# Kernel tuning notes

Hardware: AMD Instinct MI355X
Metric: run time of the kernel (lower is better)

Reference implementation:

```python
import jax, jax.numpy as jnp
import numpy as np

IN_DIM = 64
OUT_DIM = 64
NUM_HEADS = 4
NEG_SLOPE = 0.2
GAMMA = 1.0  # constraint_gamma
NUM_VARS = 100000
NUM_CLAUSES = 100000
NUM_CLUSTERS = 2048
VARS_PER = 64
CLAUSES_PER = 64
NUM_EDGES = 400000


def _xavier(k, shape):
    bound = np.sqrt(6.0 / (shape[0] + shape[1])).astype(np.float32)
    return jax.random.uniform(k, shape, jnp.float32, -bound, bound)


def setup_inputs() -> dict:
    key = jax.random.key(0)
    ks = jax.random.split(key, 11)
    return {
        "x_var": jax.random.normal(ks[0], (NUM_VARS, IN_DIM), jnp.float32),
        "x_clause": jax.random.normal(ks[1], (NUM_CLAUSES, IN_DIM), jnp.float32),
        "var_clause_edge_index": jax.random.randint(ks[2], (2, NUM_EDGES), 0, NUM_VARS),
        "edge_polarity": jax.random.normal(ks[3], (NUM_EDGES, 1), jnp.float32),
        "cluster_var_ids": jax.random.randint(ks[4], (NUM_CLUSTERS, VARS_PER), 0, NUM_VARS),
        "cluster_clause_ids": jax.random.randint(ks[5], (NUM_CLUSTERS, CLAUSES_PER), 0, NUM_CLAUSES),
        "satisfaction_scores": jax.random.uniform(ks[6], (NUM_CLAUSES,), jnp.float32),
        "active_heads": 4,
        "W_Q": _xavier(ks[7], (OUT_DIM, IN_DIM)),
        "W_K": _xavier(ks[8], (OUT_DIM, IN_DIM)),
        "W_V": _xavier(ks[9], (OUT_DIM, IN_DIM)),
        "head_weights": jnp.ones((NUM_HEADS,), jnp.float32),
        "out_proj_w": _xavier(ks[10], (OUT_DIM, OUT_DIM)),
        "out_proj_b": jnp.zeros((OUT_DIM,), jnp.float32),
    }


def reference(x_var, x_clause, var_clause_edge_index, edge_polarity,
              cluster_var_ids, cluster_clause_ids, satisfaction_scores,
              active_heads, W_Q, W_K, W_V, head_weights, out_proj_w, out_proj_b):
    # NOTE: var_clause_edge_index / edge_polarity are accepted but unused,
    # matching the original forward body.
    num_vars = x_var.shape[0]
    x_all = jnp.concatenate([x_var, x_clause], axis=0)            # [N, D]
    Q = x_all @ W_Q.T
    K = x_all @ W_K.T
    V = x_all @ W_V.T

    # Block-diagonal cluster layout: [C, S] with S = VARS_PER + CLAUSES_PER
    nodes = jnp.concatenate([cluster_var_ids, cluster_clause_ids + num_vars], axis=1)
    Qc = Q[nodes]                                                 # [C, S, D]
    Kc = K[nodes]
    Vc = V[nodes]

    scale = jnp.asarray(np.sqrt(OUT_DIM), Qc.dtype)
    scores = jnp.einsum('csd,ctd->cst', Qc, Kc) / scale            # [C, S, S]
    # constraint-aware bias on clause columns (added before leaky_relu)
    bias = jnp.concatenate(
        [jnp.zeros(cluster_var_ids.shape, scores.dtype),
         GAMMA * satisfaction_scores[cluster_clause_ids]], axis=1)  # [C, S]
    scores = jax.nn.leaky_relu(scores + bias[:, None, :], NEG_SLOPE)
    attn = jax.nn.softmax(scores, axis=-1)

    head_w = jnp.mean(head_weights[:active_heads])
    h = jnp.einsum('cst,ctd->csd', attn, Vc) * head_w             # [C, S, D]

    flat = nodes.reshape(-1)
    out = jnp.zeros_like(x_all).at[flat].add(h.reshape(-1, OUT_DIM))
    count = jnp.zeros((x_all.shape[0],), x_all.dtype).at[flat].add(1.0)
    out = out / jnp.maximum(count, 1.0)[:, None]
    out = out @ out_proj_w.T + out_proj_b

    return (x_var + out[:num_vars], x_clause + out[num_vars:])
```

## Files before the change

kernel.cpp:

```cpp
#include <hip/hip_runtime.h>


#define NV 100000
#define NN 200000
#define NCLUST 2048
#define XS 72

typedef __attribute__((ext_vector_type(8))) short short8;
typedef __attribute__((ext_vector_type(4))) unsigned uint4v;
typedef __attribute__((ext_vector_type(16))) float floatx16;

__device__ __forceinline__ unsigned short f2bf(float f) {
    union { float f; unsigned u; } v; v.f = f;
    unsigned r = v.u + 0x7fffu + ((v.u >> 16) & 1u);
    return (unsigned short)(r >> 16);
}
__device__ __forceinline__ unsigned pack2bf(float lo, float hi) {
    union { float f; unsigned u; } a, b; a.f = lo; b.f = hi;
    unsigned ra = a.u + 0x7fffu + ((a.u >> 16) & 1u);
    unsigned rb = b.u + 0x7fffu + ((b.u >> 16) & 1u);
    return (ra >> 16) | (rb & 0xffff0000u);
}
__device__ __forceinline__ int crow(int r, int lane) {
    return (r & 3) + 8 * (r >> 2) + 4 * (lane >> 5);
}

__global__ __launch_bounds__(256) void prep_kernel(
    const float* __restrict__ WQ, const float* __restrict__ WK,
    const float* __restrict__ WV, const float* __restrict__ Wout,
    const float* __restrict__ head_weights, const int* __restrict__ active_heads_p,
    unsigned short* __restrict__ Mtr, unsigned short* __restrict__ Pbf)
{
    int o = blockIdx.x * blockDim.x + threadIdx.x;
    int ah = active_heads_p[0];
    float hw = 0.f;
    for (int i = 0; i < ah; ++i) hw += head_weights[i];
    hw /= (float)ah;
    if (o < 4096) {
        int d = o >> 6, a = o & 63;
        float acc = 0.f;
        for (int j = 0; j < 64; ++j) acc += WQ[j*64 + a] * WK[j*64 + d];
        Mtr[o] = f2bf(acc * 0.125f);
    } else if (o < 8192) {
        int o2 = o - 4096;
        int j = o2 >> 6, b = o2 & 63;
        float acc = 0.f;
        for (int d = 0; d < 64; ++d) acc += Wout[j*64 + d] * WV[d*64 + b];
        Pbf[o2] = f2bf(acc * hw);
    }
}

__device__ __forceinline__ void cluster_compute(
    unsigned short* Xc, unsigned short* Eh,
    const int* ids, const float* biascl,
    const unsigned short* __restrict__ Mtr,
    unsigned short* __restrict__ accum_bf,
    int lane, int w, int m, int hk)
{
    {
        floatx16 z0 = {}, z1 = {};
        #pragma unroll
        for (int ks = 0; ks < 4; ++ks) {
            short8 mb0 = *(const short8*)(Mtr + m * 64 + ks * 16 + hk);
            short8 mb1 = *(const short8*)(Mtr + (32 + m) * 64 + ks * 16 + hk);
            short8 a = *(const short8*)&Xc[(w * 32 + m) * XS + ks * 16 + hk];
            z0 = __builtin_amdgcn_mfma_f32_32x32x16_bf16(a, mb0, z0, 0, 0, 0);
            z1 = __builtin_amdgcn_mfma_f32_32x32x16_bf16(a, mb1, z1, 0, 0, 0);
        }
        #pragma unroll
        for (int r = 0; r < 16; ++r) {
            int row = w * 32 + crow(r, lane);
            Eh[row * XS + m]      = f2bf(z0[r]);
            Eh[row * XS + 32 + m] = f2bf(z1[r]);
        }
    }

    floatx16 sc[4] = {{}, {}, {}, {}};
    #pragma unroll
    for (int ks = 0; ks < 4; ++ks) {
        short8 a = *(const short8*)&Eh[(w * 32 + m) * XS + ks * 16 + hk];
        #pragma unroll
        for (int nt = 0; nt < 4; ++nt) {
            short8 b = *(const short8*)&Xc[(nt * 32 + m) * XS + ks * 16 + hk];
            sc[nt] = __builtin_amdgcn_mfma_f32_32x32x16_bf16(a, b, sc[nt], 0, 0, 0);
        }
    }

    const float b2 = biascl[m], b3 = biascl[32 + m];
    #pragma unroll
    for (int r = 0; r < 16; ++r) {
        float a0 = sc[0][r], a1 = sc[1][r], a2 = sc[2][r] + b2, a3 = sc[3][r] + b3;
        a0 = a0 > 0.f ? a0 : 0.2f * a0;
        a1 = a1 > 0.f ? a1 : 0.2f * a1;
        a2 = a2 > 0.f ? a2 : 0.2f * a2;
        a3 = a3 > 0.f ? a3 : 0.2f * a3;
        a0 = __expf(a0); a1 = __expf(a1); a2 = __expf(a2); a3 = __expf(a3);
        float s4 = (a0 + a1) + (a2 + a3);
        #pragma unroll
        for (int off = 1; off < 32; off <<= 1) s4 += __shfl_xor(s4, off, 64);
        float inv = __builtin_amdgcn_rcpf(s4);
        sc[0][r] = a0 * inv; sc[1][r] = a1 * inv;
        sc[2][r] = a2 * inv; sc[3][r] = a3 * inv;
    }

    #pragma unroll
    for (int r = 0; r < 16; ++r) {
        int row = w * 32 + crow(r, lane);
        Eh[row * XS + m]      = f2bf(sc[0][r]);
        Eh[row * XS + 32 + m] = f2bf(sc[1][r]);
    }

    floatx16 g0 = {}, g1 = {};
    #pragma unroll
    for (int ks = 0; ks < 4; ++ks) {
        short8 a = *(const short8*)&Eh[(w * 32 + m) * XS + ks * 16 + hk];
        short8 b0, b1;
        #pragma unroll
        for (int j = 0; j < 8; ++j) {
            int t = ks * 16 + hk + j;
            b0[j] = (short)Xc[t * XS + m];
            b1[j] = (short)Xc[t * XS + 32 + m];
        }
        g0 = __builtin_amdgcn_mfma_f32_32x32x16_bf16(a, b0, g0, 0, 0, 0);
        g1 = __builtin_amdgcn_mfma_f32_32x32x16_bf16(a, b1, g1, 0, 0, 0);
    }

    #pragma unroll
    for (int r = 0; r < 16; ++r) {
        int row = w * 32 + crow(r, lane);
        Eh[row * XS + m]      = f2bf(sc[2][r]);
        Eh[row * XS + 32 + m] = f2bf(sc[3][r]);
    }

    #pragma unroll
    for (int ks = 0; ks < 4; ++ks) {
        short8 a = *(const short8*)&Eh[(w * 32 + m) * XS + ks * 16 + hk];
        short8 b0, b1;
        #pragma unroll
        for (int j = 0; j < 8; ++j) {
            int t = 64 + ks * 16 + hk + j;
            b0[j] = (short)Xc[t * XS + m];
            b1[j] = (short)Xc[t * XS + 32 + m];
        }
        g0 = __builtin_amdgcn_mfma_f32_32x32x16_bf16(a, b0, g0, 0, 0, 0);
        g1 = __builtin_amdgcn_mfma_f32_32x32x16_bf16(a, b1, g1, 0, 0, 0);
    }

    const bool ev = !(lane & 1);
    const int colbase = ev ? m : (31 + m);
    #pragma unroll
    for (int r = 0; r < 16; ++r) {
        int row = w * 32 + crow(r, lane);
        int nid = ids[row];
        float a0 = g0[r], a1 = g1[r];
        float t0 = __shfl_xor(a0, 1, 64);
        float t1 = __shfl_xor(a1, 1, 64);
        float lo = ev ? a0 : t1;
        float hi = ev ? t0 : a1;
        unsigned pk = (unsigned)f2bf(lo) | ((unsigned)f2bf(hi) << 16);
        unsigned long long addr =
            (unsigned long long)(accum_bf + (size_t)nid * 64 + colbase);
        asm volatile("global_atomic_pk_add_bf16 %0, %1, off"
                     :: "v"(addr), "v"(pk) : "memory");
    }
}

__global__ __launch_bounds__(256, 3) void attn_kernel(
    const float* __restrict__ x_var, const float* __restrict__ x_clause,
    const int* __restrict__ cvar, const int* __restrict__ ccl,
    const float* __restrict__ sat, const unsigned short* __restrict__ Mtr,
    unsigned short* __restrict__ accum_bf, float* __restrict__ countv)
{
    __shared__ unsigned short Xc[128 * XS];
    __shared__ unsigned short Eh[128 * XS];
    __shared__ unsigned stage4[16 * 256];
    __shared__ int   ids[128];
    __shared__ float biascl[64];

    const int tid = threadIdx.x, lane = tid & 63, w = tid >> 6;
    const int m = lane & 31, hk = (lane >> 5) * 8;
    const int c0 = blockIdx.x * 2;
    const int r = tid >> 1, half = tid & 1;

    int nid0, nid1;
    const float *src0, *src1;
    float satv0 = 0.f, satv1 = 0.f;
    if (r < 64) {
        nid0 = cvar[c0 * 64 + r];
        nid1 = cvar[c0 * 64 + 64 + r];
        src0 = x_var + (size_t)nid0 * 64;
        src1 = x_var + (size_t)nid1 * 64;
    } else {
        int cid0 = ccl[c0 * 64 + (r - 64)];
        int cid1 = ccl[c0 * 64 + r];
        nid0 = NV + cid0; nid1 = NV + cid1;
        src0 = x_clause + (size_t)cid0 * 64;
        src1 = x_clause + (size_t)cid1 * 64;
        if (half) { satv0 = sat[cid0]; satv1 = sat[cid1]; }
    }

    const float4* s40 = (const float4*)src0 + half * 8;
    const float4* s41 = (const float4*)src1 + half * 8;
    float4 v0[8], v1[8];
    #pragma unroll
    for (int i = 0; i < 8; ++i) v0[i] = s40[i];
    #pragma unroll
    for (int i = 0; i < 8; ++i) v1[i] = s41[i];

    if (!half) atomicAdd(&countv[nid0], 1.0f);

    {
        union { unsigned u[16]; short8 v[4]; } hb;
        #pragma unroll
        for (int i = 0; i < 8; ++i) {
            hb.u[2*i]   = pack2bf(v0[i].x, v0[i].y);
            hb.u[2*i+1] = pack2bf(v0[i].z, v0[i].w);
        }
        const int cb = half * 32;
        #pragma unroll
        for (int i = 0; i < 4; ++i) *(short8*)&Xc[r * XS + cb + i * 8] = hb.v[i];
    }
    #pragma unroll
    for (int i = 0; i < 8; ++i) {
        stage4[(2*i)   * 256 + tid] = pack2bf(v1[i].x, v1[i].y);
        stage4[(2*i+1) * 256 + tid] = pack2bf(v1[i].z, v1[i].w);
    }
    if (!half) ids[r] = nid0;
    if (r >= 64 && half) biascl[r - 64] = satv0;
    __syncthreads();

    cluster_compute(Xc, Eh, ids, biascl, Mtr, accum_bf, lane, w, m, hk);
    __syncthreads();

    {
        const int cb = half * 32;
        #pragma unroll
        for (int j = 0; j < 4; ++j) {
            uint4v t;
            #pragma unroll
            for (int q = 0; q < 4; ++q) t[q] = stage4[(4*j + q) * 256 + tid];
            *(uint4v*)&Xc[r * XS + cb + 8 * j] = t;
        }
    }
    if (!half) { ids[r] = nid1; atomicAdd(&countv[nid1], 1.0f); }
    if (r >= 64 && half) biascl[r - 64] = satv1;
    __syncthreads();

    cluster_compute(Xc, Eh, ids, biascl, Mtr, accum_bf, lane, w, m, hk);
}

__global__ __launch_bounds__(256, 4) void finalize_kernel(
    const float* __restrict__ x_var, const float* __restrict__ x_clause,
    const unsigned short* __restrict__ accum_bf, const float* __restrict__ countv,
    const unsigned short* __restrict__ Pbf, const float* __restrict__ bout,
    float* __restrict__ out)
{
    __shared__ float cnts[128];
    const int tid = threadIdx.x, lane = tid & 63, w = tid >> 6;
    const int base = blockIdx.x * 128;
    if (tid < 128) {
        int n = base + tid;
        cnts[tid] = (n < NN) ? countv[n] : 1.f;
    }
    __syncthreads();

    const int m = lane & 31, hk = (lane >> 5) * 8;
    short8 pb[2][4];
    #pragma unroll
    for (int nt = 0; nt < 2; ++nt)
        #pragma unroll
        for (int ks = 0; ks < 4; ++ks)
            pb[nt][ks] = *(const short8*)(Pbf + (nt * 32 + m) * 64 + ks * 16 + hk);
    const float bias0 = bout[m], bias1 = bout[32 + m];

    const unsigned short* arow = accum_bf + (size_t)(base + w * 32 + m) * 64;
    floatx16 c0 = {}, c1 = {};
    #pragma unroll
    for (int ks = 0; ks < 4; ++ks) {
        short8 a = *(const short8*)(arow + ks * 16 + hk);
        c0 = __builtin_amdgcn_mfma_f32_32x32x16_bf16(a, pb[0][ks], c0, 0, 0, 0);
        c1 = __builtin_amdgcn_mfma_f32_32x32x16_bf16(a, pb[1][ks], c1, 0, 0, 0);
    }
    #pragma unroll
    for (int r = 0; r < 16; ++r) {
        int lrow = w * 32 + crow(r, lane);
        int n = base + lrow;
        if (n < NN) {
            float inv = 1.0f / fmaxf(cnts[lrow], 1.0f);
            const float* xs = (n < NV) ? (x_var + (size_t)n * 64)
                                       : (x_clause + (size_t)(n - NV) * 64);
            out[(size_t)n * 64 + m]      = xs[m]      + c0[r] * inv + bias0;
            out[(size_t)n * 64 + 32 + m] = xs[32 + m] + c1[r] * inv + bias1;
        }
    }
}

extern "C" void kernel_launch(void* const* d_in, const int* in_sizes, int n_in,
                              void* d_out, int out_size, void* d_ws, size_t ws_size,
                              hipStream_t stream)
{
    const float* x_var        = (const float*)d_in[0];
    const float* x_clause     = (const float*)d_in[1];
    const int*   cvar         = (const int*)d_in[4];
    const int*   ccl          = (const int*)d_in[5];
    const float* sat          = (const float*)d_in[6];
    const int*   active_heads = (const int*)d_in[7];
    const float* WQ           = (const float*)d_in[8];
    const float* WK           = (const float*)d_in[9];
    const float* WV           = (const float*)d_in[10];
    const float* head_weights = (const float*)d_in[11];
    const float* Wout         = (const float*)d_in[12];
    const float* bout         = (const float*)d_in[13];

    unsigned short* accum_bf = (unsigned short*)d_ws;
    float* countv = (float*)(accum_bf + (size_t)NN * 64);
    unsigned short* Mtr = (unsigned short*)(countv + NN);
    unsigned short* Pbf = Mtr + 4096;

    hipMemsetAsync(accum_bf, 0, (size_t)NN * 64 * 2 + (size_t)NN * 4, stream);
    prep_kernel<<<32, 256, 0, stream>>>(WQ, WK, WV, Wout, head_weights, active_heads, Mtr, Pbf);
    attn_kernel<<<NCLUST / 2, 256, 0, stream>>>(x_var, x_clause, cvar, ccl, sat, Mtr, accum_bf, countv);
    finalize_kernel<<<(NN + 127) / 128, 256, 0, stream>>>(x_var, x_clause, accum_bf, countv, Pbf, bout, (float*)d_out);
}
```

Baseline: 217.5 us.

## Ping-pong LDS buffers across two clusters, drop staging buffer, double finalize tile

The attention kernel drops the separate stage4 LDS staging area. The second cluster's bf16 features are kept in registers and written into the first cluster's scratch buffer near the end of the first cluster's compute, so the two LDS buffers swap roles. This cuts shared memory per block and lets launch bounds request 4 blocks per CU instead of 3. One full __syncthreads is replaced by a lighter LDS-only barrier. The finalize kernel now handles 256 rows per block with two M-tiles per wave, which halves the grid and reuses the loaded Pbf fragments. The risk is higher register pressure from the carried vectors, which may spill at the tighter occupancy target.

```diff
diff --git a/kernel.cpp b/kernel.cpp
--- a/kernel.cpp
+++ b/kernel.cpp
@@ -7,7 +7,6 @@
 #define XS 72
 
 typedef __attribute__((ext_vector_type(8))) short short8;
-typedef __attribute__((ext_vector_type(4))) unsigned uint4v;
 typedef __attribute__((ext_vector_type(16))) float floatx16;
 
 __device__ __forceinline__ unsigned short f2bf(float f) {
@@ -23,6 +22,12 @@
 }
 __device__ __forceinline__ int crow(int r, int lane) {
     return (r & 3) + 8 * (r >> 2) + 4 * (lane >> 5);
+}
+__device__ __forceinline__ void bar_lds() {
+    __builtin_amdgcn_sched_barrier(0);
+    asm volatile("s_waitcnt lgkmcnt(0)" ::: "memory");
+    __builtin_amdgcn_s_barrier();
+    __builtin_amdgcn_sched_barrier(0);
 }
 
 __global__ __launch_bounds__(256) void prep_kernel(
@@ -50,12 +55,14 @@
     }
 }
 
+template<bool WN>
 __device__ __forceinline__ void cluster_compute(
-    unsigned short* Xc, unsigned short* Eh,
+    unsigned short* X, unsigned short* E,
     const int* ids, const float* biascl,
     const unsigned short* __restrict__ Mtr,
     unsigned short* __restrict__ accum_bf,
-    int lane, int w, int m, int hk)
+    int lane, int w, int m, int hk, int r, int cb,
+    short8 nx0, short8 nx1, short8 nx2, short8 nx3)
 {
     {
         floatx16 z0 = {}, z1 = {};
@@ -63,33 +70,33 @@
         for (int ks = 0; ks < 4; ++ks) {
             short8 mb0 = *(const short8*)(Mtr + m * 64 + ks * 16 + hk);
             short8 mb1 = *(const short8*)(Mtr + (32 + m) * 64 + ks * 16 + hk);
-            short8 a = *(const short8*)&Xc[(w * 32 + m) * XS + ks * 16 + hk];
+            short8 a = *(const short8*)&X[(w * 32 + m) * XS + ks * 16 + hk];
             z0 = __builtin_amdgcn_mfma_f32_32x32x16_bf16(a, mb0, z0, 0, 0, 0);
             z1 = __builtin_amdgcn_mfma_f32_32x32x16_bf16(a, mb1, z1, 0, 0, 0);
         }
         #pragma unroll
-        for (int r = 0; r < 16; ++r) {
-            int row = w * 32 + crow(r, lane);
-            Eh[row * XS + m]      = f2bf(z0[r]);
-            Eh[row * XS + 32 + m] = f2bf(z1[r]);
+        for (int rr = 0; rr < 16; ++rr) {
+            int row = w * 32 + crow(rr, lane);
+            E[row * XS + m]      = f2bf(z0[rr]);
+            E[row * XS + 32 + m] = f2bf(z1[rr]);
         }
     }
 
     floatx16 sc[4] = {{}, {}, {}, {}};
     #pragma unroll
     for (int ks = 0; ks < 4; ++ks) {
-        short8 a = *(const short8*)&Eh[(w * 32 + m) * XS + ks * 16 + hk];
+        short8 a = *(const short8*)&E[(w * 32 + m) * XS + ks * 16 + hk];
         #pragma unroll
         for (int nt = 0; nt < 4; ++nt) {
-            short8 b = *(const short8*)&Xc[(nt * 32 + m) * XS + ks * 16 + hk];
+            short8 b = *(const short8*)&X[(nt * 32 + m) * XS + ks * 16 + hk];
             sc[nt] = __builtin_amdgcn_mfma_f32_32x32x16_bf16(a, b, sc[nt], 0, 0, 0);
         }
     }
 
     const float b2 = biascl[m], b3 = biascl[32 + m];
     #pragma unroll
-    for (int r = 0; r < 16; ++r) {
-        float a0 = sc[0][r], a1 = sc[1][r], a2 = sc[2][r] + b2, a3 = sc[3][r] + b3;
+    for (int rr = 0; rr < 16; ++rr) {
+        float a0 = sc[0][rr], a1 = sc[1][rr], a2 = sc[2][rr] + b2, a3 = sc[3][rr] + b3;
         a0 = a0 > 0.f ? a0 : 0.2f * a0;
         a1 = a1 > 0.f ? a1 : 0.2f * a1;
         a2 = a2 > 0.f ? a2 : 0.2f * a2;
@@ -99,60 +106,67 @@
         #pragma unroll
         for (int off = 1; off < 32; off <<= 1) s4 += __shfl_xor(s4, off, 64);
         float inv = __builtin_amdgcn_rcpf(s4);
-        sc[0][r] = a0 * inv; sc[1][r] = a1 * inv;
-        sc[2][r] = a2 * inv; sc[3][r] = a3 * inv;
-    }
-
-    #pragma unroll
-    for (int r = 0; r < 16; ++r) {
-        int row = w * 32 + crow(r, lane);
-        Eh[row * XS + m]      = f2bf(sc[0][r]);
-        Eh[row * XS + 32 + m] = f2bf(sc[1][r]);
+        sc[0][rr] = a0 * inv; sc[1][rr] = a1 * inv;
+        sc[2][rr] = a2 * inv; sc[3][rr] = a3 * inv;
+    }
+
+    #pragma unroll
+    for (int rr = 0; rr < 16; ++rr) {
+        int row = w * 32 + crow(rr, lane);
+        E[row * XS + m]      = f2bf(sc[0][rr]);
+        E[row * XS + 32 + m] = f2bf(sc[1][rr]);
     }
 
     floatx16 g0 = {}, g1 = {};
     #pragma unroll
     for (int ks = 0; ks < 4; ++ks) {
-        short8 a = *(const short8*)&Eh[(w * 32 + m) * XS + ks * 16 + hk];
+        short8 a = *(const short8*)&E[(w * 32 + m) * XS + ks * 16 + hk];
         short8 b0, b1;
         #pragma unroll
         for (int j = 0; j < 8; ++j) {
             int t = ks * 16 + hk + j;
-            b0[j] = (short)Xc[t * XS + m];
-            b1[j] = (short)Xc[t * XS + 32 + m];
+            b0[j] = (short)X[t * XS + m];
+            b1[j] = (short)X[t * XS + 32 + m];
         }
         g0 = __builtin_amdgcn_mfma_f32_32x32x16_bf16(a, b0, g0, 0, 0, 0);
         g1 = __builtin_amdgcn_mfma_f32_32x32x16_bf16(a, b1, g1, 0, 0, 0);
     }
 
     #pragma unroll
-    for (int r = 0; r < 16; ++r) {
-        int row = w * 32 + crow(r, lane);
-        Eh[row * XS + m]      = f2bf(sc[2][r]);
-        Eh[row * XS + 32 + m] = f2bf(sc[3][r]);
+    for (int rr = 0; rr < 16; ++rr) {
+        int row = w * 32 + crow(rr, lane);
+        E[row * XS + m]      = f2bf(sc[2][rr]);
+        E[row * XS + 32 + m] = f2bf(sc[3][rr]);
     }
 
     #pragma unroll
     for (int ks = 0; ks < 4; ++ks) {
-        short8 a = *(const short8*)&Eh[(w * 32 + m) * XS + ks * 16 + hk];
+        short8 a = *(const short8*)&E[(w * 32 + m) * XS + ks * 16 + hk];
         short8 b0, b1;
         #pragma unroll
         for (int j = 0; j < 8; ++j) {
             int t = 64 + ks * 16 + hk + j;
-            b0[j] = (short)Xc[t * XS + m];
-            b1[j] = (short)Xc[t * XS + 32 + m];
+            b0[j] = (short)X[t * XS + m];
+            b1[j] = (short)X[t * XS + 32 + m];
         }
         g0 = __builtin_amdgcn_mfma_f32_32x32x16_bf16(a, b0, g0, 0, 0, 0);
         g1 = __builtin_amdgcn_mfma_f32_32x32x16_bf16(a, b1, g1, 0, 0, 0);
     }
 
+    if (WN) {
+        *(short8*)&E[r * XS + cb +  0] = nx0;
+        *(short8*)&E[r * XS + cb +  8] = nx1;
+        *(short8*)&E[r * XS + cb + 16] = nx2;
+        *(short8*)&E[r * XS + cb + 24] = nx3;
+    }
+
     const bool ev = !(lane & 1);
     const int colbase = ev ? m : (31 + m);
     #pragma unroll
-    for (int r = 0; r < 16; ++r) {
-        int row = w * 32 + crow(r, lane);
+    for (int rr = 0; rr < 16; ++rr) {
+        int row = w * 32 + crow(rr, lane);
         int nid = ids[row];
-        float a0 = g0[r], a1 = g1[r];
+        float a0 = g0[rr], a1 = g1[rr];
         float t0 = __shfl_xor(a0, 1, 64);
         float t1 = __shfl_xor(a1, 1, 64);
         float lo = ev ? a0 : t1;
@@ -165,26 +179,25 @@
     }
 }
 
-__global__ __launch_bounds__(256, 3) void attn_kernel(
+__global__ __launch_bounds__(256, 4) void attn_kernel(
     const float* __restrict__ x_var, const float* __restrict__ x_clause,
     const int* __restrict__ cvar, const int* __restrict__ ccl,
     const float* __restrict__ sat, const unsigned short* __restrict__ Mtr,
     unsigned short* __restrict__ accum_bf, float* __restrict__ countv)
 {
-    __shared__ unsigned short Xc[128 * XS];
-    __shared__ unsigned short Eh[128 * XS];
-    __shared__ unsigned stage4[16 * 256];
-    __shared__ int   ids[128];
-    __shared__ float biascl[64];
+    __shared__ unsigned short bufA[128 * XS];
+    __shared__ unsigned short bufB[128 * XS];
+    __shared__ int   ids0[128], ids1[128];
+    __shared__ float bias0[64], bias1[64];
 
     const int tid = threadIdx.x, lane = tid & 63, w = tid >> 6;
     const int m = lane & 31, hk = (lane >> 5) * 8;
     const int c0 = blockIdx.x * 2;
-    const int r = tid >> 1, half = tid & 1;
+    const int r = tid >> 1, half = tid & 1, cb = half * 32;
 
     int nid0, nid1;
     const float *src0, *src1;
-    float satv0 = 0.f, satv1 = 0.f;
+    float sv0 = 0.f, sv1 = 0.f;
     if (r < 64) {
         nid0 = cvar[c0 * 64 + r];
         nid1 = cvar[c0 * 64 + 64 + r];
@@ -196,7 +209,7 @@
         nid0 = NV + cid0; nid1 = NV + cid1;
         src0 = x_clause + (size_t)cid0 * 64;
         src1 = x_clause + (size_t)cid1 * 64;
-        if (half) { satv0 = sat[cid0]; satv1 = sat[cid1]; }
+        if (half) { sv0 = sat[cid0]; sv1 = sat[cid1]; }
     }
 
     const float4* s40 = (const float4*)src0 + half * 8;
@@ -207,46 +220,41 @@
     #pragma unroll
     for (int i = 0; i < 8; ++i) v1[i] = s41[i];
 
-    if (!half) atomicAdd(&countv[nid0], 1.0f);
+    if (!half) {
+        ids0[r] = nid0; ids1[r] = nid1;
+        atomicAdd(&countv[nid0], 1.0f);
+        atomicAdd(&countv[nid1], 1.0f);
+    }
+    if (r >= 64 && half) { bias0[r - 64] = sv0; bias1[r - 64] = sv1; }
 
     {
-        union { unsigned u[16]; short8 v[4]; } hb;
+        union { unsigned u[16]; short8 v[4]; } h0;
         #pragma unroll
         for (int i = 0; i < 8; ++i) {
-            hb.u[2*i]   = pack2bf(v0[i].x, v0[i].y);
-            hb.u[2*i+1] = pack2bf(v0[i].z, v0[i].w);
-        }
-        const int cb = half * 32;
-        #pragma unroll
-        for (int i = 0; i < 4; ++i) *(short8*)&Xc[r * XS + cb + i * 8] = hb.v[i];
-    }
+            h0.u[2*i]   = pack2bf(v0[i].x, v0[i].y);
+            h0.u[2*i+1] = pack2bf(v0[i].z, v0[i].w);
+        }
+        #pragma unroll
+        for (int i = 0; i < 4; ++i) *(short8*)&bufA[r * XS + cb + i * 8] = h0.v[i];
+    }
+    union { unsigned u[16]; short8 v[4]; } h1;
     #pragma unroll
     for (int i = 0; i < 8; ++i) {
-        stage4[(2*i)   * 256 + tid] = pack2bf(v1[i].x, v1[i].y);
-        stage4[(2*i+1) * 256 + tid] = pack2bf(v1[i].z, v1[i].w);
-    }
-    if (!half) ids[r] = nid0;
-    if (r >= 64 && half) biascl[r - 64] = satv0;
-    __syncthreads();
-
-    cluster_compute(Xc, Eh, ids, biascl, Mtr, accum_bf, lane, w, m, hk);
-    __syncthreads();
-
-    {
-        const int cb = half * 32;
-        #pragma unroll
-        for (int j = 0; j < 4; ++j) {
-            uint4v t;
-            #pragma unroll
-            for (int q = 0; q < 4; ++q) t[q] = stage4[(4*j + q) * 256 + tid];
-            *(uint4v*)&Xc[r * XS + cb + 8 * j] = t;
-        }
-    }
-    if (!half) { ids[r] = nid1; atomicAdd(&countv[nid1], 1.0f); }
-    if (r >= 64 && half) biascl[r - 64] = satv1;
-    __syncthreads();
-
-    cluster_compute(Xc, Eh, ids, biascl, Mtr, accum_bf, lane, w, m, hk);
+        h1.u[2*i]   = pack2bf(v1[i].x, v1[i].y);
+        h1.u[2*i+1] = pack2bf(v1[i].z, v1[i].w);
+    }
+
+    bar_lds();
+
+    cluster_compute<true>(bufA, bufB, ids0, bias0, Mtr, accum_bf,
+                          lane, w, m, hk, r, cb,
+                          h1.v[0], h1.v[1], h1.v[2], h1.v[3]);
+
+    bar_lds();
+
+    short8 zz = {};
+    cluster_compute<false>(bufB, bufA, ids1, bias1, Mtr, accum_bf,
+                           lane, w, m, hk, r, cb, zz, zz, zz, zz);
 }
 
 __global__ __launch_bounds__(256, 4) void finalize_kernel(
@@ -255,10 +263,10 @@
     const unsigned short* __restrict__ Pbf, const float* __restrict__ bout,
     float* __restrict__ out)
 {
-    __shared__ float cnts[128];
+    __shared__ float cnts[256];
     const int tid = threadIdx.x, lane = tid & 63, w = tid >> 6;
-    const int base = blockIdx.x * 128;
-    if (tid < 128) {
+    const int base = blockIdx.x * 256;
+    {
         int n = base + tid;
         cnts[tid] = (n < NN) ? countv[n] : 1.f;
     }
@@ -273,24 +281,28 @@
             pb[nt][ks] = *(const short8*)(Pbf + (nt * 32 + m) * 64 + ks * 16 + hk);
     const float bias0 = bout[m], bias1 = bout[32 + m];
 
-    const unsigned short* arow = accum_bf + (size_t)(base + w * 32 + m) * 64;
-    floatx16 c0 = {}, c1 = {};
-    #pragma unroll
-    for (int ks = 0; ks < 4; ++ks) {
-        short8 a = *(const short8*)(arow + ks * 16 + hk);
-        c0 = __builtin_amdgcn_mfma_f32_32x32x16_bf16(a, pb[0][ks], c0, 0, 0, 0);
-        c1 = __builtin_amdgcn_mfma_f32_32x32x16_bf16(a, pb[1][ks], c1, 0, 0, 0);
-    }
-    #pragma unroll
-    for (int r = 0; r < 16; ++r) {
-        int lrow = w * 32 + crow(r, lane);
-        int n = base + lrow;
-        if (n < NN) {
-            float inv = 1.0f / fmaxf(cnts[lrow], 1.0f);
-            const float* xs = (n < NV) ? (x_var + (size_t)n * 64)
-                                       : (x_clause + (size_t)(n - NV) * 64);
-            out[(size_t)n * 64 + m]      = xs[m]      + c0[r] * inv + bias0;
-            out[(size_t)n * 64 + 32 + m] = xs[32 + m] + c1[r] * inv + bias1;
+    #pragma unroll
+    for (int tm = 0; tm < 2; ++tm) {
+        int mt = w * 2 + tm;
+        const unsigned short* arow = accum_bf + (size_t)(base + mt * 32 + m) * 64;
+        floatx16 c0 = {}, c1 = {};
+        #pragma unroll
+        for (int ks = 0; ks < 4; ++ks) {
+            short8 a = *(const short8*)(arow + ks * 16 + hk);
+            c0 = __builtin_amdgcn_mfma_f32_32x32x16_bf16(a, pb[0][ks], c0, 0, 0, 0);
+            c1 = __builtin_amdgcn_mfma_f32_32x32x16_bf16(a, pb[1][ks], c1, 0, 0, 0);
+        }
+        #pragma unroll
+        for (int rr = 0; rr < 16; ++rr) {
+            int lrow = mt * 32 + crow(rr, lane);
+            int n = base + lrow;
+            if (n < NN) {
+                float inv = 1.0f / fmaxf(cnts[lrow], 1.0f);
+                const float* xs = (n < NV) ? (x_var + (size_t)n * 64)
+                                           : (x_clause + (size_t)(n - NV) * 64);
+                out[(size_t)n * 64 + m]      = xs[m]      + c0[rr] * inv + bias0;
+                out[(size_t)n * 64 + 32 + m] = xs[32 + m] + c1[rr] * inv + bias1;
+            }
         }
     }
 }
@@ -320,5 +332,5 @@
     hipMemsetAsync(accum_bf, 0, (size_t)NN * 64 * 2 + (size_t)NN * 4, stream);
     prep_kernel<<<32, 256, 0, stream>>>(WQ, WK, WV, Wout, head_weights, active_heads, Mtr, Pbf);
     attn_kernel<<<NCLUST / 2, 256, 0, stream>>>(x_var, x_clause, cvar, ccl, sat, Mtr, accum_bf, countv);
-    finalize_kernel<<<(NN + 127) / 128, 256, 0, stream>>>(x_var, x_clause, accum_bf, countv, Pbf, bout, (float*)d_out);
-}
+    finalize_kernel<<<(NN + 255) / 256, 256, 0, stream>>>(x_var, x_clause, accum_bf, countv, Pbf, bout, (float*)d_out);
+}
```

After: 214.5 us. No clear change (-1.3%).
